# Kernel optimization log

Hardware: AMD Instinct MI355X
Metric: run time of the kernel (lower is better)

The kernel has to match this reference:

```python
import jax, jax.numpy as jnp
import numpy as np

N_NODES = 100000
N_EDGES = 1000000
N_GRAPHS = 512
HID = 64
EDIM = 32
LAYERS = 4
BN_EPS = 1e-5


def _batchnorm(x, g, b):
    # training-mode BatchNorm1d: biased batch statistics over the node axis
    m = x.mean(axis=0)
    v = jnp.var(x, axis=0)
    return (x - m) * jax.lax.rsqrt(v + BN_EPS) * g + b


def setup_inputs() -> dict:
    key = jax.random.key(0)
    ks = jax.random.split(key, 16)
    zw = 2 * HID + EDIM  # 160: cat([x_i, x_j, e_ij])
    inp = {
        "z": jax.random.randint(ks[0], (N_NODES,), 0, 100),
        "edge_index": jax.random.randint(ks[1], (2, N_EDGES), 0, N_NODES),
        "edge_attr": jax.random.normal(ks[2], (N_EDGES, EDIM), dtype=jnp.float32),
        "batch_ids": jnp.sort(jax.random.randint(ks[3], (N_NODES,), 0, N_GRAPHS)),
        "emb": jax.random.normal(ks[4], (100, HID), dtype=jnp.float32),
        "Wf": jax.random.normal(ks[5], (LAYERS, zw, HID), dtype=jnp.float32) / np.sqrt(zw),
        "bf": jnp.zeros((LAYERS, HID), jnp.float32),
        "Ws": jax.random.normal(ks[6], (LAYERS, zw, HID), dtype=jnp.float32) / np.sqrt(zw),
        "bs": jnp.zeros((LAYERS, HID), jnp.float32),
        "g_cbn": jnp.ones((LAYERS, HID), jnp.float32),
        "b_cbn": jnp.zeros((LAYERS, HID), jnp.float32),
        "g_obn": jnp.ones((LAYERS, HID), jnp.float32),
        "b_obn": jnp.zeros((LAYERS, HID), jnp.float32),
        "W1": jax.random.normal(ks[7], (HID, HID), dtype=jnp.float32) / np.sqrt(HID),
        "b1": jnp.zeros((HID,), jnp.float32),
        "W2": jax.random.normal(ks[8], (HID, 1), dtype=jnp.float32) / np.sqrt(HID),
        "b2": jnp.zeros((1,), jnp.float32),
    }
    return inp


def reference(z, edge_index, edge_attr, batch_ids, emb, Wf, bf, Ws, bs,
              g_cbn, b_cbn, g_obn, b_obn, W1, b1, W2, b2):
    src = edge_index[0]  # x_j (source)
    dst = edge_index[1]  # x_i (target / aggregation index)
    x = emb[z]  # [N, HID]
    for l in range(LAYERS):
        # CGConv message: z_e = cat([x_i, x_j, e_ij]); m = sigmoid(f(z_e)) * softplus(s(z_e))
        z_e = jnp.concatenate([x[dst], x[src], edge_attr], axis=-1)  # [E, 160]
        msg = jax.nn.sigmoid(z_e @ Wf[l] + bf[l]) * jax.nn.softplus(z_e @ Ws[l] + bs[l])
        agg = jax.ops.segment_sum(msg, dst, num_segments=N_NODES)  # [N, HID]
        agg = _batchnorm(agg, g_cbn[l], b_cbn[l])  # CGConv's internal BN
        x = agg + x  # residual
        x = _batchnorm(x, g_obn[l], b_obn[l])  # outer BatchNorm1d
        x = jax.nn.softplus(x)
    # global mean pool over graphs
    sums = jax.ops.segment_sum(x, batch_ids, num_segments=N_GRAPHS)
    cnts = jax.ops.segment_sum(jnp.ones((N_NODES,), x.dtype), batch_ids, num_segments=N_GRAPHS)
    pooled = sums / jnp.maximum(cnts, 1.0)[:, None]
    h = jax.nn.silu(pooled @ W1 + b1)  # dropout is identity in eval mode
    out = (h @ W2 + b2)[:, 0]
    return out
```

## Files before the change

kernel.cpp:

```cpp
#include <hip/hip_runtime.h>
#include <cstdint>
#include <cstddef>

#define N_NODES 100000
#define N_EDGES 1000000
#define N_GRAPHS 512
#define HID 64
#define EDIM 32
#define LAYERS 4
#define BN_EPS 1e-5

static const size_t X_OFF    = 0;
static const size_t AGG_OFF  = (size_t)N_NODES * HID * 4;
static const size_t STA_OFF  = AGG_OFF + (size_t)N_NODES * HID * 4;
static const size_t STB_OFF  = STA_OFF + 128 * 8;
static const size_t POOL_OFF = STB_OFF + 128 * 8;
static const size_t CNT_OFF  = POOL_OFF + (size_t)N_GRAPHS * HID * 4;
static const size_t P_OFF    = CNT_OFF + (size_t)N_GRAPHS * 4;

__device__ __forceinline__ float rl_f(float v, int k) {
    return __uint_as_float(__builtin_amdgcn_readlane(__float_as_uint(v), k));
}
__device__ __forceinline__ float sigmoidf_(float x) {
    return 1.f / (1.f + __expf(-x));
}
__device__ __forceinline__ float softplusf_(float x) {
    return fmaxf(x, 0.f) + __logf(1.f + __expf(-fabsf(x)));
}

__global__ __launch_bounds__(256) void cg_embed(const int* __restrict__ z,
                                                const float* __restrict__ emb,
                                                float* __restrict__ x) {
    int i = blockIdx.x * 256 + threadIdx.x;
    if (i < N_NODES * HID) {
        x[i] = emb[z[i >> 6] * HID + (i & 63)];
    }
}

__global__ __launch_bounds__(256) void cg_nodeP(const float* __restrict__ x,
                                                const float* __restrict__ Wf,
                                                const float* __restrict__ Ws,
                                                float* __restrict__ P) {
    __shared__ __align__(16) float xs[16][68];
    const int j4 = (threadIdx.x & 15) * 4;
    const int r  = threadIdx.x >> 4;
    const int base = blockIdx.x * 16;

    {
        const float4 v = *(const float4*)(x + (size_t)(base + r) * HID + j4);
        *(float4*)(&xs[r][j4]) = v;
    }
    __syncthreads();

    float4 a0 = {0, 0, 0, 0}, a1 = {0, 0, 0, 0}, a2 = {0, 0, 0, 0}, a3 = {0, 0, 0, 0};
#pragma unroll 4
    for (int k = 0; k < 64; k++) {
        float xv = xs[r][k];
        float4 w0 = *(const float4*)(Wf + (size_t)k * HID + j4);
        float4 w1 = *(const float4*)(Ws + (size_t)k * HID + j4);
        float4 w2 = *(const float4*)(Wf + (size_t)(64 + k) * HID + j4);
        float4 w3 = *(const float4*)(Ws + (size_t)(64 + k) * HID + j4);
        a0.x = fmaf(xv, w0.x, a0.x); a0.y = fmaf(xv, w0.y, a0.y);
        a0.z = fmaf(xv, w0.z, a0.z); a0.w = fmaf(xv, w0.w, a0.w);
        a1.x = fmaf(xv, w1.x, a1.x); a1.y = fmaf(xv, w1.y, a1.y);
        a1.z = fmaf(xv, w1.z, a1.z); a1.w = fmaf(xv, w1.w, a1.w);
        a2.x = fmaf(xv, w2.x, a2.x); a2.y = fmaf(xv, w2.y, a2.y);
        a2.z = fmaf(xv, w2.z, a2.z); a2.w = fmaf(xv, w2.w, a2.w);
        a3.x = fmaf(xv, w3.x, a3.x); a3.y = fmaf(xv, w3.y, a3.y);
        a3.z = fmaf(xv, w3.z, a3.z); a3.w = fmaf(xv, w3.w, a3.w);
    }
    float* o = P + (size_t)(base + r) * 256;
    *(float4*)(o + 0   + j4) = a0;
    *(float4*)(o + 64  + j4) = a1;
    *(float4*)(o + 128 + j4) = a2;
    *(float4*)(o + 192 + j4) = a3;
}

__global__ __launch_bounds__(256) void cg_edge(const float* __restrict__ P,
                                               const int* __restrict__ ei,
                                               const float* __restrict__ ea,
                                               const float* __restrict__ WfE,
                                               const float* __restrict__ WsE,
                                               const float* __restrict__ bf,
                                               const float* __restrict__ bs,
                                               float* __restrict__ agg) {
    const int j = threadIdx.x & 63;
    float wfe[EDIM], wse[EDIM];
#pragma unroll
    for (int k = 0; k < EDIM; k++) {
        wfe[k] = WfE[k * HID + j];
        wse[k] = WsE[k * HID + j];
    }
    const float bfv = bf[j], bsv = bs[j];
    const int wave = blockIdx.x * 4 + (threadIdx.x >> 6);
    const int nwaves = gridDim.x * 4;

    int e = wave;
    int eu = __builtin_amdgcn_readfirstlane(e);
    int ps = ei[eu];
    int pd = ei[N_EDGES + eu];
    float per = ea[(size_t)eu * EDIM + (j & 31)];

    for (; e < N_EDGES; e += nwaves) {
        const int srcn = ps, dstn = pd;
        const float er = per;
        const int ne = e + nwaves;
        if (ne < N_EDGES) {
            const int neu = __builtin_amdgcn_readfirstlane(ne);
            ps = ei[neu];
            pd = ei[N_EDGES + neu];
            per = ea[(size_t)neu * EDIM + (j & 31)];
        }
        const size_t db = (size_t)dstn * 256, sb = (size_t)srcn * 256;
        const float pf0 = P[db + j];
        const float pf1 = P[sb + 128 + j];
        const float ps0 = P[db + 64 + j];
        const float ps1 = P[sb + 192 + j];
        float uf = bfv, us = bsv;
#pragma unroll
        for (int k = 0; k < EDIM; k++) {
            const float ek = rl_f(er, k);
            uf = fmaf(ek, wfe[k], uf);
            us = fmaf(ek, wse[k], us);
        }
        uf += pf0 + pf1;
        us += ps0 + ps1;
        const float m = sigmoidf_(uf) * softplusf_(us);
        unsafeAtomicAdd(&agg[(size_t)dstn * HID + j], m);
    }
}

__global__ __launch_bounds__(256) void cg_stats(const float* __restrict__ a,
                                                double* __restrict__ st) {
    const int j = threadIdx.x & 63, rl = threadIdx.x >> 6;
    float s = 0.f, q = 0.f;
    for (int n = blockIdx.x * 4 + rl; n < N_NODES; n += gridDim.x * 4) {
        float v = a[(size_t)n * HID + j];
        s += v;
        q += v * v;
    }
    __shared__ float ls[4][64], lq[4][64];
    ls[rl][j] = s;
    lq[rl][j] = q;
    __syncthreads();
    if (threadIdx.x < 64) {
        float S = ls[0][j] + ls[1][j] + ls[2][j] + ls[3][j];
        float Q = lq[0][j] + lq[1][j] + lq[2][j] + lq[3][j];
        unsafeAtomicAdd(&st[j], (double)S);
        unsafeAtomicAdd(&st[64 + j], (double)Q);
    }
}

__global__ __launch_bounds__(256) void cg_bn1res(float* __restrict__ agg,
                                                 const float* __restrict__ x,
                                                 const float* __restrict__ g,
                                                 const float* __restrict__ b,
                                                 const double* __restrict__ stA,
                                                 double* __restrict__ stB) {
    const int j = threadIdx.x & 63, rl = threadIdx.x >> 6;
    const double mean = stA[j] * (1.0 / N_NODES);
    const double var  = stA[64 + j] * (1.0 / N_NODES) - mean * mean;
    const float sc = (float)((double)g[j] / sqrt(var + BN_EPS));
    const float sh = (float)((double)b[j] - mean * (double)sc);
    float s = 0.f, q = 0.f;
    for (int n = blockIdx.x * 4 + rl; n < N_NODES; n += gridDim.x * 4) {
        size_t idx = (size_t)n * HID + j;
        float v = fmaf(agg[idx], sc, sh) + x[idx];
        agg[idx] = v;
        s += v;
        q += v * v;
    }
    __shared__ float ls[4][64], lq[4][64];
    ls[rl][j] = s;
    lq[rl][j] = q;
    __syncthreads();
    if (threadIdx.x < 64) {
        float S = ls[0][j] + ls[1][j] + ls[2][j] + ls[3][j];
        float Q = lq[0][j] + lq[1][j] + lq[2][j] + lq[3][j];
        unsafeAtomicAdd(&stB[j], (double)S);
        unsafeAtomicAdd(&stB[64 + j], (double)Q);
    }
}

__global__ __launch_bounds__(256) void cg_bn2act(const float* __restrict__ agg,
                                                 float* __restrict__ x,
                                                 const float* __restrict__ g,
                                                 const float* __restrict__ b,
                                                 const double* __restrict__ stB) {
    const int j = threadIdx.x & 63, rl = threadIdx.x >> 6;
    const double mean = stB[j] * (1.0 / N_NODES);
    const double var  = stB[64 + j] * (1.0 / N_NODES) - mean * mean;
    const float sc = (float)((double)g[j] / sqrt(var + BN_EPS));
    const float sh = (float)((double)b[j] - mean * (double)sc);
    for (int n = blockIdx.x * 4 + rl; n < N_NODES; n += gridDim.x * 4) {
        size_t idx = (size_t)n * HID + j;
        x[idx] = softplusf_(fmaf(agg[idx], sc, sh));
    }
}

__global__ __launch_bounds__(256) void cg_pool(const float* __restrict__ x,
                                               const int* __restrict__ bid,
                                               float* __restrict__ pooled,
                                               float* __restrict__ cnt) {
    const int j = threadIdx.x & 63, rl = threadIdx.x >> 6;
    const int chunk = (N_NODES + gridDim.x - 1) / gridDim.x;
    const int s0 = blockIdx.x * chunk;
    const int e0 = min(s0 + chunk, N_NODES);
    float acc = 0.f, c = 0.f;
    int cur = -1;
    for (int n = s0 + rl; n < e0; n += 4) {
        int bg = bid[n];
        if (bg != cur) {
            if (cur >= 0) {
                unsafeAtomicAdd(&pooled[(size_t)cur * HID + j], acc);
                if (j == 0) unsafeAtomicAdd(&cnt[cur], c);
            }
            cur = bg;
            acc = 0.f;
            c = 0.f;
        }
        acc += x[(size_t)n * HID + j];
        c += 1.f;
    }
    if (cur >= 0) {
        unsafeAtomicAdd(&pooled[(size_t)cur * HID + j], acc);
        if (j == 0) unsafeAtomicAdd(&cnt[cur], c);
    }
}

__global__ __launch_bounds__(64) void cg_mlp(const float* __restrict__ pooled,
                                             const float* __restrict__ cnt,
                                             const float* __restrict__ W1,
                                             const float* __restrict__ b1,
                                             const float* __restrict__ W2,
                                             const float* __restrict__ b2,
                                             float* __restrict__ out) {
    const int g = blockIdx.x;
    const int j = threadIdx.x;
    const float c = fmaxf(cnt[g], 1.f);
    const float p = pooled[(size_t)g * HID + j] / c;
    float h = b1[j];
    for (int k = 0; k < HID; k++) {
        h = fmaf(rl_f(p, k), W1[k * HID + j], h);
    }
    const float hs = h * sigmoidf_(h);
    float v = hs * W2[j];
#pragma unroll
    for (int off = 32; off > 0; off >>= 1) v += __shfl_down(v, off);
    if (j == 0) out[g] = v + b2[0];
}

extern "C" void kernel_launch(void* const* d_in, const int* in_sizes, int n_in,
                              void* d_out, int out_size, void* d_ws, size_t ws_size,
                              hipStream_t stream) {
    const int*   z   = (const int*)d_in[0];
    const int*   ei  = (const int*)d_in[1];
    const float* ea  = (const float*)d_in[2];
    const int*   bid = (const int*)d_in[3];
    const float* emb = (const float*)d_in[4];
    const float* Wf  = (const float*)d_in[5];
    const float* bf  = (const float*)d_in[6];
    const float* Ws  = (const float*)d_in[7];
    const float* bs  = (const float*)d_in[8];
    const float* gc  = (const float*)d_in[9];
    const float* bc  = (const float*)d_in[10];
    const float* go  = (const float*)d_in[11];
    const float* bo  = (const float*)d_in[12];
    const float* W1  = (const float*)d_in[13];
    const float* b1  = (const float*)d_in[14];
    const float* W2  = (const float*)d_in[15];
    const float* b2  = (const float*)d_in[16];
    float* out = (float*)d_out;

    char* ws = (char*)d_ws;
    float*  x      = (float*)(ws + X_OFF);
    float*  agg    = (float*)(ws + AGG_OFF);
    double* stA    = (double*)(ws + STA_OFF);
    double* stB    = (double*)(ws + STB_OFF);
    float*  pooled = (float*)(ws + POOL_OFF);
    float*  cnt    = (float*)(ws + CNT_OFF);
    float*  P      = (float*)(ws + P_OFF);

    cg_embed<<<(N_NODES * HID + 255) / 256, 256, 0, stream>>>(z, emb, x);

    for (int l = 0; l < LAYERS; l++) {
        const float* Wfl = Wf + (size_t)l * 160 * HID;
        const float* Wsl = Ws + (size_t)l * 160 * HID;
        hipMemsetAsync(ws + AGG_OFF, 0, (size_t)N_NODES * HID * 4 + 2048, stream);
        cg_nodeP<<<N_NODES / 16, 256, 0, stream>>>(x, Wfl, Wsl, P);
        cg_edge<<<4096, 256, 0, stream>>>(P, ei, ea, Wfl + 128 * HID, Wsl + 128 * HID,
                                          bf + l * HID, bs + l * HID, agg);
        cg_stats<<<1024, 256, 0, stream>>>(agg, stA);
        cg_bn1res<<<1024, 256, 0, stream>>>(agg, x, gc + l * HID, bc + l * HID, stA, stB);
        cg_bn2act<<<1024, 256, 0, stream>>>(agg, x, go + l * HID, bo + l * HID, stB);
    }

    hipMemsetAsync(ws + POOL_OFF, 0, (size_t)N_GRAPHS * HID * 4 + N_GRAPHS * 4, stream);
    cg_pool<<<1024, 256, 0, stream>>>(x, bid, pooled, cnt);
    cg_mlp<<<N_GRAPHS, 64, 0, stream>>>(pooled, cnt, W1, b1, W2, b2, out);
}
```

Before: 2.525 ms.

## Sort edges by destination (CSR) and accumulate messages per node before atomics

Builds a destination-sorted edge permutation once per call (histogram, single-block scan, atomic scatter). The edge kernel then walks contiguous chunks of sorted edges, keeps the destination's P rows in registers, and accumulates messages locally, issuing one atomic per destination run instead of one per edge. The node projection kernel is also retiled to process 64 nodes per block for better weight reuse. The cost is three extra preprocessing kernels with a serial 1024-thread scan, plus indirect gathers through perm for source indices and edge attributes.

Result: no change. 2.493 ms (-1.3%).

```diff
diff --git a/kernel.cpp b/kernel.cpp
--- a/kernel.cpp
+++ b/kernel.cpp
@@ -11,12 +11,16 @@
 #define BN_EPS 1e-5
 
 static const size_t X_OFF    = 0;
-static const size_t AGG_OFF  = (size_t)N_NODES * HID * 4;
-static const size_t STA_OFF  = AGG_OFF + (size_t)N_NODES * HID * 4;
-static const size_t STB_OFF  = STA_OFF + 128 * 8;
-static const size_t POOL_OFF = STB_OFF + 128 * 8;
-static const size_t CNT_OFF  = POOL_OFF + (size_t)N_GRAPHS * HID * 4;
-static const size_t P_OFF    = CNT_OFF + (size_t)N_GRAPHS * 4;
+static const size_t AGG_OFF  = X_OFF + 25600000;
+static const size_t STA_OFF  = AGG_OFF + 25600000;
+static const size_t STB_OFF  = STA_OFF + 1024;
+static const size_t POOL_OFF = STB_OFF + 1024;
+static const size_t CNT_OFF  = POOL_OFF + 131072;
+static const size_t DEG_OFF  = CNT_OFF + 2048;
+static const size_t ECUR_OFF = DEG_OFF + 400128;
+static const size_t PERM_OFF = ECUR_OFF + 400128;
+static const size_t DSTS_OFF = PERM_OFF + 4000000;
+static const size_t P_OFF    = DSTS_OFF + 4000000;
 
 __device__ __forceinline__ float rl_f(float v, int k) {
     return __uint_as_float(__builtin_amdgcn_readlane(__float_as_uint(v), k));
@@ -26,6 +30,12 @@
 }
 __device__ __forceinline__ float softplusf_(float x) {
     return fmaxf(x, 0.f) + __logf(1.f + __expf(-fabsf(x)));
+}
+__device__ __forceinline__ void fma4(float4& a, const float4& wv, float xv) {
+    a.x = fmaf(xv, wv.x, a.x);
+    a.y = fmaf(xv, wv.y, a.y);
+    a.z = fmaf(xv, wv.z, a.z);
+    a.w = fmaf(xv, wv.w, a.w);
 }
 
 __global__ __launch_bounds__(256) void cg_embed(const int* __restrict__ z,
@@ -37,53 +47,116 @@
     }
 }
 
-__global__ __launch_bounds__(256) void cg_nodeP(const float* __restrict__ x,
-                                                const float* __restrict__ Wf,
-                                                const float* __restrict__ Ws,
-                                                float* __restrict__ P) {
-    __shared__ __align__(16) float xs[16][68];
-    const int j4 = (threadIdx.x & 15) * 4;
-    const int r  = threadIdx.x >> 4;
-    const int base = blockIdx.x * 16;
-
-    {
-        const float4 v = *(const float4*)(x + (size_t)(base + r) * HID + j4);
-        *(float4*)(&xs[r][j4]) = v;
-    }
+__global__ __launch_bounds__(256) void cg_hist(const int* __restrict__ ei,
+                                               int* __restrict__ deg) {
+    int e = blockIdx.x * 256 + threadIdx.x;
+    if (e < N_EDGES) atomicAdd(&deg[ei[N_EDGES + e]], 1);
+}
+
+#define SPAN 98
+__global__ __launch_bounds__(1024) void cg_scan(const int* __restrict__ deg,
+                                                int* __restrict__ ecur) {
+    __shared__ int ps[1024];
+    const int t = threadIdx.x;
+    const int s0 = t * SPAN;
+    int sum = 0;
+    for (int i = 0; i < SPAN; i++) {
+        int idx = s0 + i;
+        if (idx < N_NODES) sum += deg[idx];
+    }
+    ps[t] = sum;
     __syncthreads();
-
-    float4 a0 = {0, 0, 0, 0}, a1 = {0, 0, 0, 0}, a2 = {0, 0, 0, 0}, a3 = {0, 0, 0, 0};
-#pragma unroll 4
+    for (int off = 1; off < 1024; off <<= 1) {
+        int v = (t >= off) ? ps[t - off] : 0;
+        __syncthreads();
+        ps[t] += v;
+        __syncthreads();
+    }
+    int run = ps[t] - sum;
+    for (int i = 0; i < SPAN; i++) {
+        int idx = s0 + i;
+        if (idx < N_NODES) {
+            ecur[idx] = run;
+            run += deg[idx];
+        }
+    }
+}
+
+__global__ __launch_bounds__(256) void cg_scatter(const int* __restrict__ ei,
+                                                  int* __restrict__ ecur,
+                                                  int* __restrict__ perm,
+                                                  int* __restrict__ dst_s) {
+    int e = blockIdx.x * 256 + threadIdx.x;
+    if (e < N_EDGES) {
+        int d = ei[N_EDGES + e];
+        int pos = atomicAdd(&ecur[d], 1);
+        perm[pos] = e;
+        dst_s[pos] = d;
+    }
+}
+
+__global__ __launch_bounds__(256) void cg_nodeP4(const float* __restrict__ x,
+                                                 const float* __restrict__ Wf,
+                                                 const float* __restrict__ Ws,
+                                                 float* __restrict__ P) {
+    __shared__ __align__(16) float xs[64][68];
+    const int tid = threadIdx.x;
+    const int base = blockIdx.x * 64;
+#pragma unroll
+    for (int i = 0; i < 4; i++) {
+        int f4 = tid * 4 + i;
+        int r = f4 >> 4, c4 = (f4 & 15) * 4;
+        float4 v = {0, 0, 0, 0};
+        if (base + r < N_NODES) v = *(const float4*)(x + (size_t)(base + r) * HID + c4);
+        *(float4*)(&xs[r][c4]) = v;
+    }
+    __syncthreads();
+
+    const int c = tid & 15, g = tid >> 4;
+    const int j4 = c * 4;
+    float4 acc[4][4];
+#pragma unroll
+    for (int m = 0; m < 4; m++)
+#pragma unroll
+        for (int q = 0; q < 4; q++) acc[m][q] = {0, 0, 0, 0};
+
     for (int k = 0; k < 64; k++) {
-        float xv = xs[r][k];
         float4 w0 = *(const float4*)(Wf + (size_t)k * HID + j4);
         float4 w1 = *(const float4*)(Ws + (size_t)k * HID + j4);
         float4 w2 = *(const float4*)(Wf + (size_t)(64 + k) * HID + j4);
         float4 w3 = *(const float4*)(Ws + (size_t)(64 + k) * HID + j4);
-        a0.x = fmaf(xv, w0.x, a0.x); a0.y = fmaf(xv, w0.y, a0.y);
-        a0.z = fmaf(xv, w0.z, a0.z); a0.w = fmaf(xv, w0.w, a0.w);
-        a1.x = fmaf(xv, w1.x, a1.x); a1.y = fmaf(xv, w1.y, a1.y);
-        a1.z = fmaf(xv, w1.z, a1.z); a1.w = fmaf(xv, w1.w, a1.w);
-        a2.x = fmaf(xv, w2.x, a2.x); a2.y = fmaf(xv, w2.y, a2.y);
-        a2.z = fmaf(xv, w2.z, a2.z); a2.w = fmaf(xv, w2.w, a2.w);
-        a3.x = fmaf(xv, w3.x, a3.x); a3.y = fmaf(xv, w3.y, a3.y);
-        a3.z = fmaf(xv, w3.z, a3.z); a3.w = fmaf(xv, w3.w, a3.w);
-    }
-    float* o = P + (size_t)(base + r) * 256;
-    *(float4*)(o + 0   + j4) = a0;
-    *(float4*)(o + 64  + j4) = a1;
-    *(float4*)(o + 128 + j4) = a2;
-    *(float4*)(o + 192 + j4) = a3;
-}
-
-__global__ __launch_bounds__(256) void cg_edge(const float* __restrict__ P,
-                                               const int* __restrict__ ei,
-                                               const float* __restrict__ ea,
-                                               const float* __restrict__ WfE,
-                                               const float* __restrict__ WsE,
-                                               const float* __restrict__ bf,
-                                               const float* __restrict__ bs,
-                                               float* __restrict__ agg) {
+#pragma unroll
+        for (int m = 0; m < 4; m++) {
+            float xv = xs[g + m * 16][k];
+            fma4(acc[m][0], w0, xv);
+            fma4(acc[m][1], w1, xv);
+            fma4(acc[m][2], w2, xv);
+            fma4(acc[m][3], w3, xv);
+        }
+    }
+#pragma unroll
+    for (int m = 0; m < 4; m++) {
+        int r = base + g + m * 16;
+        if (r < N_NODES) {
+            float* o = P + (size_t)r * 256;
+            *(float4*)(o + j4)       = acc[m][0];
+            *(float4*)(o + 64 + j4)  = acc[m][1];
+            *(float4*)(o + 128 + j4) = acc[m][2];
+            *(float4*)(o + 192 + j4) = acc[m][3];
+        }
+    }
+}
+
+__global__ __launch_bounds__(256) void cg_edge2(const float* __restrict__ P,
+                                                const int* __restrict__ ei,
+                                                const float* __restrict__ ea,
+                                                const int* __restrict__ perm,
+                                                const int* __restrict__ dst_s,
+                                                const float* __restrict__ WfE,
+                                                const float* __restrict__ WsE,
+                                                const float* __restrict__ bf,
+                                                const float* __restrict__ bs,
+                                                float* __restrict__ agg) {
     const int j = threadIdx.x & 63;
     float wfe[EDIM], wse[EDIM];
 #pragma unroll
@@ -93,29 +166,42 @@
     }
     const float bfv = bf[j], bsv = bs[j];
     const int wave = blockIdx.x * 4 + (threadIdx.x >> 6);
-    const int nwaves = gridDim.x * 4;
-
-    int e = wave;
-    int eu = __builtin_amdgcn_readfirstlane(e);
-    int ps = ei[eu];
-    int pd = ei[N_EDGES + eu];
-    float per = ea[(size_t)eu * EDIM + (j & 31)];
-
-    for (; e < N_EDGES; e += nwaves) {
-        const int srcn = ps, dstn = pd;
-        const float er = per;
-        const int ne = e + nwaves;
-        if (ne < N_EDGES) {
-            const int neu = __builtin_amdgcn_readfirstlane(ne);
-            ps = ei[neu];
-            pd = ei[N_EDGES + neu];
-            per = ea[(size_t)neu * EDIM + (j & 31)];
-        }
-        const size_t db = (size_t)dstn * 256, sb = (size_t)srcn * 256;
-        const float pf0 = P[db + j];
-        const float pf1 = P[sb + 128 + j];
-        const float ps0 = P[db + 64 + j];
-        const float ps1 = P[sb + 192 + j];
+    const int nw = gridDim.x * 4;
+    const int chunk = (N_EDGES + nw - 1) / nw;
+    const int e0 = wave * chunk;
+    const int e1 = min(e0 + chunk, N_EDGES);
+    if (e0 >= e1) return;
+
+    int eu = __builtin_amdgcn_readfirstlane(e0);
+    int d_c  = dst_s[eu];
+    int pe_c = perm[eu];
+    int s_c  = ei[pe_c];
+    float er_c = ea[(size_t)pe_c * EDIM + (j & 31)];
+
+    int cur = d_c;
+    float pf0 = P[(size_t)cur * 256 + j];
+    float ps0 = P[(size_t)cur * 256 + 64 + j];
+    float acc = 0.f;
+
+    for (int e = e0; e < e1; ++e) {
+        const int d = d_c, srcn = s_c;
+        const float er = er_c;
+        if (e + 1 < e1) {
+            int nu = __builtin_amdgcn_readfirstlane(e + 1);
+            d_c  = dst_s[nu];
+            pe_c = perm[nu];
+            s_c  = ei[pe_c];
+            er_c = ea[(size_t)pe_c * EDIM + (j & 31)];
+        }
+        if (d != cur) {
+            unsafeAtomicAdd(&agg[(size_t)cur * HID + j], acc);
+            acc = 0.f;
+            cur = d;
+            pf0 = P[(size_t)cur * 256 + j];
+            ps0 = P[(size_t)cur * 256 + 64 + j];
+        }
+        const float sf = P[(size_t)srcn * 256 + 128 + j];
+        const float ss = P[(size_t)srcn * 256 + 192 + j];
         float uf = bfv, us = bsv;
 #pragma unroll
         for (int k = 0; k < EDIM; k++) {
@@ -123,11 +209,11 @@
             uf = fmaf(ek, wfe[k], uf);
             us = fmaf(ek, wse[k], us);
         }
-        uf += pf0 + pf1;
-        us += ps0 + ps1;
-        const float m = sigmoidf_(uf) * softplusf_(us);
-        unsafeAtomicAdd(&agg[(size_t)dstn * HID + j], m);
-    }
+        uf += pf0 + sf;
+        us += ps0 + ss;
+        acc += sigmoidf_(uf) * softplusf_(us);
+    }
+    unsafeAtomicAdd(&agg[(size_t)cur * HID + j], acc);
 }
 
 __global__ __launch_bounds__(256) void cg_stats(const float* __restrict__ a,
@@ -279,23 +365,33 @@
     double* stB    = (double*)(ws + STB_OFF);
     float*  pooled = (float*)(ws + POOL_OFF);
     float*  cnt    = (float*)(ws + CNT_OFF);
+    int*    deg    = (int*)(ws + DEG_OFF);
+    int*    ecur   = (int*)(ws + ECUR_OFF);
+    int*    perm   = (int*)(ws + PERM_OFF);
+    int*    dst_s  = (int*)(ws + DSTS_OFF);
     float*  P      = (float*)(ws + P_OFF);
+
+    (void)hipMemsetAsync(ws + DEG_OFF, 0, 400000, stream);
+    cg_hist<<<(N_EDGES + 255) / 256, 256, 0, stream>>>(ei, deg);
+    cg_scan<<<1, 1024, 0, stream>>>(deg, ecur);
+    cg_scatter<<<(N_EDGES + 255) / 256, 256, 0, stream>>>(ei, ecur, perm, dst_s);
 
     cg_embed<<<(N_NODES * HID + 255) / 256, 256, 0, stream>>>(z, emb, x);
 
     for (int l = 0; l < LAYERS; l++) {
         const float* Wfl = Wf + (size_t)l * 160 * HID;
         const float* Wsl = Ws + (size_t)l * 160 * HID;
-        hipMemsetAsync(ws + AGG_OFF, 0, (size_t)N_NODES * HID * 4 + 2048, stream);
-        cg_nodeP<<<N_NODES / 16, 256, 0, stream>>>(x, Wfl, Wsl, P);
-        cg_edge<<<4096, 256, 0, stream>>>(P, ei, ea, Wfl + 128 * HID, Wsl + 128 * HID,
-                                          bf + l * HID, bs + l * HID, agg);
+        (void)hipMemsetAsync(ws + AGG_OFF, 0, 25600000 + 2048, stream);
+        cg_nodeP4<<<(N_NODES + 63) / 64, 256, 0, stream>>>(x, Wfl, Wsl, P);
+        cg_edge2<<<4096, 256, 0, stream>>>(P, ei, ea, perm, dst_s,
+                                           Wfl + 128 * HID, Wsl + 128 * HID,
+                                           bf + l * HID, bs + l * HID, agg);
         cg_stats<<<1024, 256, 0, stream>>>(agg, stA);
         cg_bn1res<<<1024, 256, 0, stream>>>(agg, x, gc + l * HID, bc + l * HID, stA, stB);
         cg_bn2act<<<1024, 256, 0, stream>>>(agg, x, go + l * HID, bo + l * HID, stB);
     }
 
-    hipMemsetAsync(ws + POOL_OFF, 0, (size_t)N_GRAPHS * HID * 4 + N_GRAPHS * 4, stream);
+    (void)hipMemsetAsync(ws + POOL_OFF, 0, 131072 + 2048, stream);
     cg_pool<<<1024, 256, 0, stream>>>(x, bid, pooled, cnt);
     cg_mlp<<<N_GRAPHS, 64, 0, stream>>>(pooled, cnt, W1, b1, W2, b2, out);
 }
```
